# Optimization experiments

Measured on AMD Instinct MI355X. Metric: run time of the kernel, lower is better.

The kernel has to match this reference:

```python
import jax, jax.numpy as jnp
import numpy as np

B, L, DIM = 16, 1024, 768
HEADS, DIM_HEAD = 12, 64
INNER = HEADS * DIM_HEAD  # 768


def _make_perm(key, l, dim):
    # first `dim` entries identity, rest a random permutation of [dim, l*dim)
    tail = dim + jax.random.permutation(key, (l - 1) * dim)
    return jnp.concatenate([jnp.arange(dim), tail]).astype(jnp.int32)


def setup_inputs() -> dict:
    key = jax.random.key(0)
    kx, kq, kk, kv, ko, kp1, kp2 = jax.random.split(key, 7)
    s = DIM ** -0.5
    return {
        "x": jax.random.normal(kx, (B, L, DIM), dtype=jnp.float32),
        "Wq": jax.random.normal(kq, (DIM, INNER), dtype=jnp.float32) * s,
        "Wk": jax.random.normal(kk, (DIM, INNER), dtype=jnp.float32) * s,
        "Wv": jax.random.normal(kv, (DIM, INNER), dtype=jnp.float32) * s,
        "Wo": jax.random.normal(ko, (INNER, DIM), dtype=jnp.float32) * (INNER ** -0.5),
        "bo": jnp.zeros((DIM,), dtype=jnp.float32),
        "permq": _make_perm(kp1, L, DIM),
        "permk": _make_perm(kp2, L, DIM),
    }


def reference(x, Wq, Wk, Wv, Wo, bo, permq, permk):
    b, l, d = x.shape
    scale = DIM_HEAD ** -0.5
    flat = x.reshape(b, l * d)
    xq = flat[:, permq].reshape(b, l, d)  # irregular gather across (seq*dim)
    xk = flat[:, permk].reshape(b, l, d)
    # projections + head split: b n (h d) -> b h n d
    q = (xq @ Wq).reshape(b, l, HEADS, DIM_HEAD).transpose(0, 2, 1, 3)
    k = (xk @ Wk).reshape(b, l, HEADS, DIM_HEAD).transpose(0, 2, 1, 3)
    v = (x @ Wv).reshape(b, l, HEADS, DIM_HEAD).transpose(0, 2, 1, 3)
    dots = jnp.einsum('bhnd,bhmd->bhnm', q, k) * scale
    attn = jax.nn.softmax(dots, axis=-1)
    out = jnp.einsum('bhnm,bhmd->bhnd', attn, v)
    out = out.transpose(0, 2, 1, 3).reshape(b, l, INNER)
    return out @ Wo + bo
```

## Files before the change

kernel.cpp:

```cpp
#include <hip/hip_runtime.h>

typedef unsigned short u16;
typedef __attribute__((ext_vector_type(8))) short bf16x8;
typedef __attribute__((ext_vector_type(4))) float f32x4;
typedef __attribute__((ext_vector_type(16))) float f32x16;

#define MFMA16(a, b, c) __builtin_amdgcn_mfma_f32_16x16x32_bf16(a, b, c, 0, 0, 0)
#define MFMA32(a, b, c) __builtin_amdgcn_mfma_f32_32x32x16_bf16(a, b, c, 0, 0, 0)

#if defined(__has_builtin)
# if __has_builtin(__builtin_amdgcn_cvt_pk_bf16_f32)
#  define HAS_CVT_PK 1
# else
#  define HAS_CVT_PK 0
# endif
#else
# define HAS_CVT_PK 0
#endif

__device__ __forceinline__ u16 f2b(float f) {
    union { float f; unsigned int u; } v;
    v.f = f;
    unsigned int u = v.u;
    return (u16)((u + 0x7fffu + ((u >> 16) & 1u)) >> 16);
}

__device__ __forceinline__ unsigned int f2b_pk(float a, float b) {
#if HAS_CVT_PK
    auto r = __builtin_amdgcn_cvt_pk_bf16_f32(a, b);
    unsigned int u;
    __builtin_memcpy(&u, &r, 4);
    return u;
#else
    return (unsigned int)f2b(a) | ((unsigned int)f2b(b) << 16);
#endif
}

__device__ __forceinline__ void g2l16(const u16* gsrc, u16* ldst) {
    __builtin_amdgcn_global_load_lds(
        (const __attribute__((address_space(1))) void*)gsrc,
        (__attribute__((address_space(3))) void*)ldst,
        16, 0, 0);
}

__global__ __launch_bounds__(256) void prep_weights(
    const float* __restrict__ Wq, const float* __restrict__ Wk,
    const float* __restrict__ Wv, const float* __restrict__ Wo,
    u16* __restrict__ wqt, u16* __restrict__ wkt,
    u16* __restrict__ wvt, u16* __restrict__ wot) {
    int id = blockIdx.x * 256 + threadIdx.x;
    int k = id / 768, n = id % 768;
    int t = n * 768 + k;
    wqt[t] = f2b(Wq[id] * (0.125f * 1.44269504088896340736f));
    wkt[t] = f2b(Wk[id]);
    wvt[t] = f2b(Wv[id]);
    wot[t] = f2b(Wo[id]);
}

__global__ __launch_bounds__(256) void cast_transpose(
    const float* __restrict__ x, u16* __restrict__ xb, u16* __restrict__ xT) {
    __shared__ __attribute__((aligned(16))) u16 T[16 * 1032];
    int t = threadIdx.x;
    int j0 = blockIdx.x * 1024;
#pragma unroll
    for (int b = 0; b < 16; ++b) {
        float4 v = *(const float4*)&x[(size_t)b * 786432 + j0 + 4 * t];
        uint2 o = make_uint2(f2b_pk(v.x, v.y), f2b_pk(v.z, v.w));
        *(uint2*)&T[b * 1032 + 4 * t] = o;
        *(uint2*)&xb[(size_t)b * 786432 + j0 + 4 * t] = o;
    }
    __syncthreads();
#pragma unroll
    for (int p = 0; p < 4; ++p) {
        int jl = t + 256 * p;
        union { u16 u[16]; int4 v[2]; } r;
#pragma unroll
        for (int b = 0; b < 16; ++b) r.u[b] = T[b * 1032 + jl];
        size_t base = (size_t)(j0 + jl) * 16;
        *(int4*)&xT[base] = r.v[0];
        *(int4*)&xT[base + 8] = r.v[1];
    }
}

__global__ __launch_bounds__(256) void gather_rows(
    const u16* __restrict__ xT, const int* __restrict__ permq,
    const int* __restrict__ permk, u16* __restrict__ xqT,
    u16* __restrict__ xkT) {
    int j = blockIdx.x * 256 + threadIdx.x;
    int pq = permq[j], pk = permk[j];
    const int4* sq = (const int4*)&xT[(size_t)pq * 16];
    const int4* sk = (const int4*)&xT[(size_t)pk * 16];
    int4 q0 = sq[0], q1 = sq[1];
    int4 k0 = sk[0], k1 = sk[1];
    int4* dq = (int4*)&xqT[(size_t)j * 16];
    int4* dk = (int4*)&xkT[(size_t)j * 16];
    dq[0] = q0; dq[1] = q1;
    dk[0] = k0; dk[1] = k1;
}

__global__ __launch_bounds__(256) void untranspose(
    const u16* __restrict__ srcQ, const u16* __restrict__ srcK,
    u16* __restrict__ dstQ, u16* __restrict__ dstK) {
    __shared__ u16 T[16 * 1034];
    const u16* src = blockIdx.y ? srcK : srcQ;
    u16* dst = blockIdx.y ? dstK : dstQ;
    int t = threadIdx.x;
    int j0 = blockIdx.x * 1024;
#pragma unroll
    for (int p = 0; p < 8; ++p) {
        int c = p * 256 + t;
        union { u16 u[8]; int4 v; } r;
        r.v = *(const int4*)&src[(size_t)j0 * 16 + c * 8];
        int jl = c >> 1, h = (c & 1) * 8;
#pragma unroll
        for (int w = 0; w < 8; ++w) T[(h + w) * 1034 + jl] = r.u[w];
    }
    __syncthreads();
#pragma unroll
    for (int b = 0; b < 16; ++b) {
        const unsigned int* s = (const unsigned int*)&T[b * 1034 + 4 * t];
        uint2 o = make_uint2(s[0], s[1]);
        *(uint2*)&dst[(size_t)b * 786432 + j0 + 4 * t] = o;
    }
}

__device__ __forceinline__ void gemm_core(
    const u16* __restrict__ A, const u16* __restrict__ Bt,
    u16* __restrict__ Cb, float* __restrict__ Cf,
    const float* __restrict__ bias, int M, int K, int N, int mode) {
    __shared__ __attribute__((aligned(16))) u16 As[128 * 32];
    __shared__ __attribute__((aligned(16))) u16 Bs[128 * 32];
    int tid = threadIdx.x;
    int m0 = blockIdx.y * 128, n0 = blockIdx.x * 128;
    int wave = tid >> 6, lane = tid & 63;
    int lo = lane & 15, quad = lane >> 4;
    int wm = (wave >> 1) * 64, wn = (wave & 1) * 64;
    f32x4 acc[4][4] = {};

    int c0 = wave * 64 + lane;
    int c1 = 256 + c0;
    const u16* pA0 = A + (size_t)(m0 + (c0 >> 2)) * K + (c0 & 3) * 8;
    const u16* pA1 = A + (size_t)(m0 + (c1 >> 2)) * K + (c1 & 3) * 8;
    const u16* pB0 = Bt + (size_t)(n0 + (c0 >> 2)) * K + (c0 & 3) * 8;
    const u16* pB1 = Bt + (size_t)(n0 + (c1 >> 2)) * K + (c1 & 3) * 8;
    u16* lA0 = &As[(wave * 64) * 8];
    u16* lA1 = &As[(256 + wave * 64) * 8];
    u16* lB0 = &Bs[(wave * 64) * 8];
    u16* lB1 = &Bs[(256 + wave * 64) * 8];

    for (int k0 = 0; k0 < K; k0 += 32) {
        __syncthreads();
        g2l16(pA0, lA0); g2l16(pA1, lA1);
        g2l16(pB0, lB0); g2l16(pB1, lB1);
        pA0 += 32; pA1 += 32; pB0 += 32; pB1 += 32;
        __syncthreads();
        bf16x8 af[4], bf[4];
#pragma unroll
        for (int mi = 0; mi < 4; ++mi)
            af[mi] = *(const bf16x8*)&As[(wm + mi * 16 + lo) * 32 + quad * 8];
#pragma unroll
        for (int nj = 0; nj < 4; ++nj)
            bf[nj] = *(const bf16x8*)&Bs[(wn + nj * 16 + lo) * 32 + quad * 8];
#pragma unroll
        for (int mi = 0; mi < 4; ++mi)
#pragma unroll
            for (int nj = 0; nj < 4; ++nj)
                acc[mi][nj] = MFMA16(af[mi], bf[nj], acc[mi][nj]);
    }
#pragma unroll
    for (int mi = 0; mi < 4; ++mi)
#pragma unroll
        for (int nj = 0; nj < 4; ++nj) {
            int col = n0 + wn + nj * 16 + lo;
#pragma unroll
            for (int r = 0; r < 4; ++r) {
                int row = m0 + wm + mi * 16 + quad * 4 + r;
                float v = acc[mi][nj][r];
                if (mode) Cf[(size_t)row * N + col] = v + bias[col];
                else      Cb[(size_t)row * N + col] = f2b(v);
            }
        }
}

__global__ __launch_bounds__(256) void gemm_qkv(
    const u16* __restrict__ xqb, const u16* __restrict__ wqt, u16* __restrict__ Qb,
    const u16* __restrict__ xkb, const u16* __restrict__ wkt, u16* __restrict__ Kb,
    const u16* __restrict__ xb,  const u16* __restrict__ wvt, u16* __restrict__ Vb) {
    int z = blockIdx.z;
    const u16* A = (z == 0) ? xqb : (z == 1) ? xkb : xb;
    const u16* W = (z == 0) ? wqt : (z == 1) ? wkt : wvt;
    u16* C = (z == 0) ? Qb : (z == 1) ? Kb : Vb;
    gemm_core(A, W, C, nullptr, nullptr, 16384, 768, 768, 0);
}

__global__ __launch_bounds__(256) void gemm_out(
    const u16* __restrict__ A, const u16* __restrict__ Bt,
    float* __restrict__ Cf, const float* __restrict__ bias) {
    gemm_core(A, Bt, nullptr, Cf, bias, 16384, 768, 768, 1);
}

#define LDA 72
__global__ __launch_bounds__(256) void transpose_v(
    const u16* __restrict__ Vb, u16* __restrict__ Vt) {
    __shared__ __attribute__((aligned(16))) u16 tile[64 * LDA];
    int lt = blockIdx.x;
    int bh = blockIdx.y;
    int b = bh / 12, h = bh % 12;
    int tid = threadIdx.x;
    int row = tid >> 3, co = (tid & 7) * 8;
#pragma unroll
    for (int p = 0; p < 2; ++p) {
        int r2 = row + p * 32;
        *(int4*)&tile[r2 * LDA + co] =
            *(const int4*)&Vb[(size_t)(b * 1024 + lt * 64 + r2) * 768 + h * 64 + co];
    }
    __syncthreads();
    int d = tid >> 2, nc = (tid & 3) * 16;
    union { u16 u[16]; int4 v[2]; } tt;
#pragma unroll
    for (int j = 0; j < 16; ++j) {
        int pp = nc + j;
        int col = (pp & 1) * 32 + (pp >> 1);
        tt.u[j] = tile[col * LDA + d];
    }
    size_t base = ((size_t)bh * 64 + d) * 1024 + lt * 64 + nc;
    *(int4*)&Vt[base] = tt.v[0];
    *(int4*)&Vt[base + 8] = tt.v[1];
}

#define LDK 72
#define LDP 72
__global__ __launch_bounds__(256) void flash_attn(
    const u16* __restrict__ Qb, const u16* __restrict__ Kb,
    const u16* __restrict__ Vt, u16* __restrict__ AO) {
    __shared__ __attribute__((aligned(16))) u16 Ks[64 * LDK];
    __shared__ __attribute__((aligned(16))) u16 Vs[64 * LDK];
    __shared__ __attribute__((aligned(16))) u16 Ps[128 * LDP];
    int id = blockIdx.x;
    int bh = (id & 7) + ((id >> 6) << 3);
    int qt = (id >> 3) & 7;
    int b = bh / 12, h = bh % 12;
    int tid = threadIdx.x, wave = tid >> 6, lane = tid & 63;
    int ln = lane & 31, hi = lane >> 5;
    int q0 = qt * 128;

    bf16x8 qa[4];
    {
        const u16* qrow = &Qb[(size_t)(b * 1024 + q0 + wave * 32 + ln) * 768 + h * 64 + hi * 8];
#pragma unroll
        for (int kk = 0; kk < 4; ++kk)
            qa[kk] = *(const bf16x8*)&qrow[kk * 16];
    }

    const float M2 = 24.0f;
    float l_part[16] = {};
    f32x16 acc_o[2] = {};
    const size_t kbase = (size_t)b * 1024 * 768 + h * 64;
    const size_t vbase = (size_t)bh * 64 * 1024;
    int srow = tid >> 3, sco = (tid & 7) * 8;

    int4 kr0 = *(const int4*)&Kb[kbase + (size_t)srow * 768 + sco];
    int4 kr1 = *(const int4*)&Kb[kbase + (size_t)(srow + 32) * 768 + sco];
    int4 vr0 = *(const int4*)&Vt[vbase + (size_t)srow * 1024 + sco];
    int4 vr1 = *(const int4*)&Vt[vbase + (size_t)(srow + 32) * 1024 + sco];

    for (int t = 0; t < 16; ++t) {
        __syncthreads();
        *(int4*)&Ks[srow * LDK + sco] = kr0;
        *(int4*)&Ks[(srow + 32) * LDK + sco] = kr1;
        *(int4*)&Vs[srow * LDK + sco] = vr0;
        *(int4*)&Vs[(srow + 32) * LDK + sco] = vr1;
        __syncthreads();
        int tn = (t + 1) & 15;
        kr0 = *(const int4*)&Kb[kbase + (size_t)(tn * 64 + srow) * 768 + sco];
        kr1 = *(const int4*)&Kb[kbase + (size_t)(tn * 64 + srow + 32) * 768 + sco];
        vr0 = *(const int4*)&Vt[vbase + (size_t)srow * 1024 + tn * 64 + sco];
        vr1 = *(const int4*)&Vt[vbase + (size_t)(srow + 32) * 1024 + tn * 64 + sco];
        f32x16 sacc[2] = {};
#pragma unroll
        for (int nj = 0; nj < 2; ++nj)
#pragma unroll
            for (int kk = 0; kk < 4; ++kk) {
                bf16x8 kb = *(const bf16x8*)&Ks[(ln + 32 * nj) * LDK + kk * 16 + hi * 8];
                sacc[nj] = MFMA32(qa[kk], kb, sacc[nj]);
            }
        int pbase = (wave * 32 + 4 * hi) * LDP + 2 * ln;
#pragma unroll
        for (int g = 0; g < 4; ++g)
#pragma unroll
            for (int r = 0; r < 4; ++r) {
                float p0 = __builtin_amdgcn_exp2f(sacc[0][4 * g + r] - M2);
                float p1 = __builtin_amdgcn_exp2f(sacc[1][4 * g + r] - M2);
                l_part[4 * g + r] += p0 + p1;
                *(unsigned int*)&Ps[pbase + (8 * g + r) * LDP] = f2b_pk(p0, p1);
            }
#pragma unroll
        for (int nk = 0; nk < 4; ++nk) {
            bf16x8 pa = *(const bf16x8*)&Ps[(wave * 32 + ln) * LDP + nk * 16 + hi * 8];
#pragma unroll
            for (int njd = 0; njd < 2; ++njd) {
                bf16x8 vb = *(const bf16x8*)&Vs[(ln + 32 * njd) * LDK + nk * 16 + hi * 8];
                acc_o[njd] = MFMA32(pa, vb, acc_o[njd]);
            }
        }
    }
#pragma unroll
    for (int r = 0; r < 16; ++r) {
        float s = l_part[r];
#pragma unroll
        for (int off = 1; off <= 16; off <<= 1) s += __shfl_xor(s, off, 64);
        float inv = 1.0f / s;
        int row = b * 1024 + q0 + wave * 32 + (r & 3) + 8 * (r >> 2) + 4 * hi;
#pragma unroll
        for (int njd = 0; njd < 2; ++njd)
            AO[(size_t)row * 768 + h * 64 + ln + 32 * njd] = f2b(acc_o[njd][r] * inv);
    }
}

static const size_t SZ_W  = (size_t)768 * 768 * 2;
static const size_t SZ_X  = (size_t)16 * 1024 * 768 * 2;
static const size_t OFF_WQT = 0;
static const size_t OFF_WKT = SZ_W;
static const size_t OFF_WVT = 2 * SZ_W;
static const size_t OFF_WOT = 3 * SZ_W;
static const size_t OFF_XB  = 4 * SZ_W;
static const size_t OFF_XQB = OFF_XB  + SZ_X;
static const size_t OFF_XKB = OFF_XQB + SZ_X;
static const size_t OFF_QB  = OFF_XKB + SZ_X;
static const size_t OFF_KB  = OFF_QB  + SZ_X;
static const size_t OFF_VB  = OFF_KB  + SZ_X;
static const size_t OFF_XT  = OFF_QB;
static const size_t OFF_XQT = OFF_KB;
static const size_t OFF_XKT = OFF_VB;
static const size_t OFF_VT  = OFF_XQB;
static const size_t OFF_AO  = OFF_XKB;

extern "C" void kernel_launch(void* const* d_in, const int* in_sizes, int n_in,
                              void* d_out, int out_size, void* d_ws, size_t ws_size,
                              hipStream_t stream) {
    const float* x  = (const float*)d_in[0];
    const float* Wq = (const float*)d_in[1];
    const float* Wk = (const float*)d_in[2];
    const float* Wv = (const float*)d_in[3];
    const float* Wo = (const float*)d_in[4];
    const float* bo = (const float*)d_in[5];
    const int* permq = (const int*)d_in[6];
    const int* permk = (const int*)d_in[7];
    float* out = (float*)d_out;
    char* ws = (char*)d_ws;
    u16* wqt = (u16*)(ws + OFF_WQT);
    u16* wkt = (u16*)(ws + OFF_WKT);
    u16* wvt = (u16*)(ws + OFF_WVT);
    u16* wot = (u16*)(ws + OFF_WOT);
    u16* xb  = (u16*)(ws + OFF_XB);
    u16* xqb = (u16*)(ws + OFF_XQB);
    u16* xkb = (u16*)(ws + OFF_XKB);
    u16* Qb  = (u16*)(ws + OFF_QB);
    u16* Kb  = (u16*)(ws + OFF_KB);
    u16* Vb  = (u16*)(ws + OFF_VB);
    u16* xT  = (u16*)(ws + OFF_XT);
    u16* xqT = (u16*)(ws + OFF_XQT);
    u16* xkT = (u16*)(ws + OFF_XKT);
    u16* Vt  = (u16*)(ws + OFF_VT);
    u16* AO  = (u16*)(ws + OFF_AO);

    prep_weights<<<2304, 256, 0, stream>>>(Wq, Wk, Wv, Wo, wqt, wkt, wvt, wot);
    cast_transpose<<<768, 256, 0, stream>>>(x, xb, xT);
    gather_rows<<<3072, 256, 0, stream>>>(xT, permq, permk, xqT, xkT);
    untranspose<<<dim3(768, 2), 256, 0, stream>>>(xqT, xkT, xqb, xkb);
    gemm_qkv<<<dim3(6, 128, 3), 256, 0, stream>>>(xqb, wqt, Qb, xkb, wkt, Kb, xb, wvt, Vb);
    transpose_v<<<dim3(16, 192), 256, 0, stream>>>(Vb, Vt);
    flash_attn<<<1536, 256, 0, stream>>>(Qb, Kb, Vt, AO);
    gemm_out<<<dim3(6, 128), 256, 0, stream>>>(AO, wot, out, bo);
}
```

Before: 401.9 us.

## Keep softmax probabilities in registers via transposed QK MFMA and permlane swaps

The QK^T MFMA operands are swapped so each lane holds scores for a single query row. The probabilities are then packed to bf16 and rearranged with v_permlane32_swap straight into the A-operand layout for the PV MFMA, so the LDS round-trip through the Ps buffer and its reads and writes are gone. The row-sum reduction shrinks to one cross-half shuffle, and the V transpose no longer interleaves columns because the key ordering now matches directly. The change relies on gfx950-specific inline asm and a careful layout correspondence, and it may raise register pressure.

Measured after the change: 391.8 us. -2.5%, faster.

```diff
diff --git a/kernel.cpp b/kernel.cpp
--- a/kernel.cpp
+++ b/kernel.cpp
@@ -34,6 +34,12 @@
 #else
     return (unsigned int)f2b(a) | ((unsigned int)f2b(b) << 16);
 #endif
+}
+
+__device__ __forceinline__ unsigned int cvtpk_asm(float a, float b) {
+    unsigned int r;
+    asm("v_cvt_pk_bf16_f32 %0, %1, %2" : "=v"(r) : "v"(a), "v"(b));
+    return r;
 }
 
 __device__ __forceinline__ void g2l16(const u16* gsrc, u16* ldst) {
@@ -218,24 +224,19 @@
     int d = tid >> 2, nc = (tid & 3) * 16;
     union { u16 u[16]; int4 v[2]; } tt;
 #pragma unroll
-    for (int j = 0; j < 16; ++j) {
-        int pp = nc + j;
-        int col = (pp & 1) * 32 + (pp >> 1);
-        tt.u[j] = tile[col * LDA + d];
-    }
+    for (int j = 0; j < 16; ++j)
+        tt.u[j] = tile[(nc + j) * LDA + d];
     size_t base = ((size_t)bh * 64 + d) * 1024 + lt * 64 + nc;
     *(int4*)&Vt[base] = tt.v[0];
     *(int4*)&Vt[base + 8] = tt.v[1];
 }
 
 #define LDK 72
-#define LDP 72
 __global__ __launch_bounds__(256) void flash_attn(
     const u16* __restrict__ Qb, const u16* __restrict__ Kb,
     const u16* __restrict__ Vt, u16* __restrict__ AO) {
     __shared__ __attribute__((aligned(16))) u16 Ks[64 * LDK];
     __shared__ __attribute__((aligned(16))) u16 Vs[64 * LDK];
-    __shared__ __attribute__((aligned(16))) u16 Ps[128 * LDP];
     int id = blockIdx.x;
     int bh = (id & 7) + ((id >> 6) << 3);
     int qt = (id >> 3) & 7;
@@ -253,7 +254,7 @@
     }
 
     const float M2 = 24.0f;
-    float l_part[16] = {};
+    float l_own = 0.0f;
     f32x16 acc_o[2] = {};
     const size_t kbase = (size_t)b * 1024 * 768 + h * 64;
     const size_t vbase = (size_t)bh * 64 * 1024;
@@ -282,38 +283,49 @@
 #pragma unroll
             for (int kk = 0; kk < 4; ++kk) {
                 bf16x8 kb = *(const bf16x8*)&Ks[(ln + 32 * nj) * LDK + kk * 16 + hi * 8];
-                sacc[nj] = MFMA32(qa[kk], kb, sacc[nj]);
+                sacc[nj] = MFMA32(kb, qa[kk], sacc[nj]);
             }
-        int pbase = (wave * 32 + 4 * hi) * LDP + 2 * ln;
-#pragma unroll
-        for (int g = 0; g < 4; ++g)
-#pragma unroll
-            for (int r = 0; r < 4; ++r) {
-                float p0 = __builtin_amdgcn_exp2f(sacc[0][4 * g + r] - M2);
-                float p1 = __builtin_amdgcn_exp2f(sacc[1][4 * g + r] - M2);
-                l_part[4 * g + r] += p0 + p1;
-                *(unsigned int*)&Ps[pbase + (8 * g + r) * LDP] = f2b_pk(p0, p1);
+#pragma unroll
+        for (int nj = 0; nj < 2; ++nj) {
+            float p[16];
+#pragma unroll
+            for (int r = 0; r < 16; ++r)
+                p[r] = __builtin_amdgcn_exp2f(sacc[nj][r] - M2);
+            l_own += (((p[0] + p[1]) + (p[2] + p[3])) + ((p[4] + p[5]) + (p[6] + p[7])))
+                   + (((p[8] + p[9]) + (p[10] + p[11])) + ((p[12] + p[13]) + (p[14] + p[15])));
+            unsigned int c[8];
+#pragma unroll
+            for (int m = 0; m < 8; ++m)
+                c[m] = cvtpk_asm(p[2 * m], p[2 * m + 1]);
+            asm("v_permlane32_swap_b32 %0, %1" : "+v"(c[0]), "+v"(c[2]));
+            asm("v_permlane32_swap_b32 %0, %1" : "+v"(c[1]), "+v"(c[3]));
+            asm("v_permlane32_swap_b32 %0, %1" : "+v"(c[4]), "+v"(c[6]));
+            asm("v_permlane32_swap_b32 %0, %1" : "+v"(c[5]), "+v"(c[7]));
+            union { unsigned int w[4]; bf16x8 v; } pa0, pa1;
+            pa0.w[0] = c[0]; pa0.w[1] = c[1]; pa0.w[2] = c[2]; pa0.w[3] = c[3];
+            pa1.w[0] = c[4]; pa1.w[1] = c[5]; pa1.w[2] = c[6]; pa1.w[3] = c[7];
+#pragma unroll
+            for (int njd = 0; njd < 2; ++njd) {
+                bf16x8 vb0 = *(const bf16x8*)&Vs[(ln + 32 * njd) * LDK + (2 * nj) * 16 + hi * 8];
+                acc_o[njd] = MFMA32(pa0.v, vb0, acc_o[njd]);
             }
 #pragma unroll
-        for (int nk = 0; nk < 4; ++nk) {
-            bf16x8 pa = *(const bf16x8*)&Ps[(wave * 32 + ln) * LDP + nk * 16 + hi * 8];
-#pragma unroll
             for (int njd = 0; njd < 2; ++njd) {
-                bf16x8 vb = *(const bf16x8*)&Vs[(ln + 32 * njd) * LDK + nk * 16 + hi * 8];
-                acc_o[njd] = MFMA32(pa, vb, acc_o[njd]);
+                bf16x8 vb1 = *(const bf16x8*)&Vs[(ln + 32 * njd) * LDK + (2 * nj + 1) * 16 + hi * 8];
+                acc_o[njd] = MFMA32(pa1.v, vb1, acc_o[njd]);
             }
         }
     }
+    float l = l_own + __shfl_xor(l_own, 32, 64);
+    float inv = 1.0f / l;
 #pragma unroll
     for (int r = 0; r < 16; ++r) {
-        float s = l_part[r];
-#pragma unroll
-        for (int off = 1; off <= 16; off <<= 1) s += __shfl_xor(s, off, 64);
-        float inv = 1.0f / s;
-        int row = b * 1024 + q0 + wave * 32 + (r & 3) + 8 * (r >> 2) + 4 * hi;
+        int qrow = (r & 3) + 8 * (r >> 2) + 4 * hi;
+        float invq = __shfl(inv, qrow, 64);
+        int row = b * 1024 + q0 + wave * 32 + qrow;
 #pragma unroll
         for (int njd = 0; njd < 2; ++njd)
-            AO[(size_t)row * 768 + h * 64 + ln + 32 * njd] = f2b(acc_o[njd][r] * inv);
+            AO[(size_t)row * 768 + h * 64 + ln + 32 * njd] = f2b(acc_o[njd][r] * invq);
     }
 }
 
```
